# Performance work log

Measured on AMD Instinct MI355X. Metric: run time of the kernel, lower is better.

## Reference

```python
import jax, jax.numpy as jnp
import numpy as np

B, WK, HRS = 2048, 52, 8760
DT = 0.125          # Euler step in days (3-hourly), exactly representable
RANGE_PRED = 7      # forecast horizon in days


def setup_inputs() -> dict:
    key = jax.random.key(0)
    k1, k2, k3, k4 = jax.random.split(key, 4)
    # X_in: [B, weeks, 5, 1]; channel 0 = start time in days (same across batch,
    # the torch code reads X_in[0, week, 0, 0]); channels 1..4 = N,P,Z,D init.
    X_in = jax.random.uniform(k1, (B, WK, 5, 1), jnp.float32, 0.1, 3.0)
    t0 = jnp.arange(WK, dtype=jnp.float32) * 7.0
    X_in = X_in.at[:, :, 0, 0].set(jnp.broadcast_to(t0, (B, WK)))
    global_f = jax.random.uniform(k2, (B, HRS), jnp.float32)          # light forcing in [0,1]
    global_m = jax.random.uniform(k3, (B, HRS), jnp.float32) * 0.1    # mixing rate, small
    params_value = jax.random.uniform(k4, (B, 10), jnp.float32, 0.1, 1.0)
    return {"X_in": X_in, "global_f": global_f, "global_m": global_m,
            "params_value": params_value, "dt": DT, "range_pred": RANGE_PRED}


def reference(X_in, global_f, global_m, params_value, dt, range_pred):
    # Fixed multipliers from the torch code
    pv = jnp.asarray([1.0, 2.0, 0.1, 0.05, 0.1, 0.3, 0.6, 0.15, 0.4, 0.1], X_in.dtype)
    Q0, Vm, thr = 8.0, 1.0, 0.01  # Q0 = 4 + 2.5 + 1.5 + 0
    chi, rho, gam, lam, eps, alp, bet, eta, phi, zet = [params_value[:, i][:, None] for i in range(10)]  # [B,1]

    n_steps = int(round(range_pred / dt))      # 56
    stride = int(round(1.0 / dt))              # 8 -> daily sampling of output

    # Hourly forcing gather: same time axis for every batch element (torch uses X_in[0,...])
    t0 = X_in[0, :, 0, 0]                                                     # [W]
    times = t0[:, None] + jnp.arange(n_steps + 1, dtype=X_in.dtype) * dt      # [W, S]
    idx = jnp.round(times * 24.0).astype(jnp.int32)
    f = jnp.take(global_f, idx, axis=1)[:, :, :n_steps]                       # [B, W, T]
    m = jnp.take(global_m, idx, axis=1)[:, :, :n_steps]

    def step(carry, ft_mt):
        N, P, Z, D = carry                      # each [B, W]
        ft, mt = ft_mt
        Pc = jnp.maximum(thr, P)
        Zc = jnp.maximum(thr, Z)
        gN = N / (chi * pv[0] + N)
        zg = rho * pv[1] * (1.0 - jnp.exp(-lam * pv[3] * Pc)) * Zc
        up = Vm * gN * ft * Pc
        Nn = N + dt * (-up + alp * pv[5] * zg + eps * pv[4] * P + gam * pv[2] * Z + phi * pv[8] * D + mt * (Q0 - N))
        Pn = P + dt * (up - zg - eps * pv[4] * P - eta * pv[7] * P - mt * P)
        Zn = Z + dt * (bet * pv[6] * zg - gam * pv[2] * Z - mt * Z)
        Dn = D + dt * (eta * pv[7] * P + (1.0 - alp * pv[5] - bet * pv[6]) * zg - phi * pv[8] * D - zet * pv[9] * D - mt * D)
        new = (Nn, Pn, Zn, Dn)
        return new, jnp.stack(new, axis=0)      # [4, B, W]

    carry0 = (X_in[:, :, 1, 0], X_in[:, :, 2, 0], X_in[:, :, 3, 0], X_in[:, :, 4, 0])
    _, ys = jax.lax.scan(step, carry0, (jnp.moveaxis(f, 2, 0), jnp.moveaxis(m, 2, 0)))  # ys: [T, 4, B, W]
    traj = jnp.concatenate([jnp.stack(carry0, axis=0)[None], ys], axis=0)               # [S, 4, B, W]
    out = jnp.moveaxis(traj, (0, 1), (3, 2))                                            # [B, W, 4, S]
    return out[:, :, :, ::stride]               # daily samples: [B, W, 4, range_pred+1]
```

## Files before the change

### kernel.cpp

```cpp
#include <hip/hip_runtime.h>
#include <hip/hip_bf16.h>


#define NPZD_B 2048
#define NPZD_WK 52
#define NPZD_HRS 8760
#define NPZD_NSTEPS 56

__global__ __launch_bounds__(64) void npzd_kernel(
    const float* __restrict__ X_in,
    const float* __restrict__ gf,
    const float* __restrict__ gm,
    const float* __restrict__ params,
    const float* __restrict__ dt_ptr,
    float* __restrict__ out)
{
    const int t = blockIdx.x * blockDim.x + threadIdx.x;
    if (t >= NPZD_B * NPZD_WK) return;
    const int b = t / NPZD_WK;
    const int w = t - b * NPZD_WK;

    const float t0w = X_in[(size_t)w * 5];
    const int idx0 = (int)rintf(t0w * 24.0f);
    const float* __restrict__ frow = gf + (size_t)b * NPZD_HRS + idx0;
    const float* __restrict__ mrow = gm + (size_t)b * NPZD_HRS + idx0;

    float fv[NPZD_NSTEPS], mv[NPZD_NSTEPS];
    #pragma unroll
    for (int i = 0; i < NPZD_NSTEPS; ++i) fv[i] = frow[3 * i];
    #pragma unroll
    for (int i = 0; i < NPZD_NSTEPS; ++i) mv[i] = mrow[3 * i];

    const float dt = dt_ptr[0];

    const float* xb = X_in + (size_t)t * 5;
    float N = xb[1], P = xb[2], Z = xb[3], D = xb[4];

    const float* pp = params + (size_t)b * 10;
    const float chi   = pp[0];
    const float rho2  = pp[1] * 2.0f;
    const float gam1  = pp[2] * 0.1f;
    const float lam05 = pp[3] * 0.05f;
    const float eps1  = pp[4] * 0.1f;
    const float alp3  = pp[5] * 0.3f;
    const float bet6  = pp[6] * 0.6f;
    const float eta15 = pp[7] * 0.15f;
    const float phi4  = pp[8] * 0.4f;
    const float zet1  = pp[9] * 0.1f;
    const float rem   = 1.0f - alp3 - bet6;

    float oN[8], oP[8], oZ[8], oD[8];
    oN[0] = N; oP[0] = P; oZ[0] = Z; oD[0] = D;

    #pragma unroll
    for (int s = 0; s < NPZD_NSTEPS; ++s) {
        const float ft = fv[s], mt = mv[s];
        const float Pc = fmaxf(0.01f, P);
        const float Zc = fmaxf(0.01f, Z);
        const float gN = N / (chi + N);
        const float zg = rho2 * (1.0f - __expf(-lam05 * Pc)) * Zc;
        const float up = gN * ft * Pc;
        const float Nn = N + dt * (-up + alp3 * zg + eps1 * P + gam1 * Z + phi4 * D + mt * (8.0f - N));
        const float Pn = P + dt * (up - zg - eps1 * P - eta15 * P - mt * P);
        const float Zn = Z + dt * (bet6 * zg - gam1 * Z - mt * Z);
        const float Dn = D + dt * (eta15 * P + rem * zg - phi4 * D - zet1 * D - mt * D);
        N = Nn; P = Pn; Z = Zn; D = Dn;
        if ((s & 7) == 7) {
            const int c = (s >> 3) + 1;
            oN[c] = N; oP[c] = P; oZ[c] = Z; oD[c] = D;
        }
    }

    float4* o4 = (float4*)(out + (size_t)t * 32);
    o4[0] = make_float4(oN[0], oN[1], oN[2], oN[3]);
    o4[1] = make_float4(oN[4], oN[5], oN[6], oN[7]);
    o4[2] = make_float4(oP[0], oP[1], oP[2], oP[3]);
    o4[3] = make_float4(oP[4], oP[5], oP[6], oP[7]);
    o4[4] = make_float4(oZ[0], oZ[1], oZ[2], oZ[3]);
    o4[5] = make_float4(oZ[4], oZ[5], oZ[6], oZ[7]);
    o4[6] = make_float4(oD[0], oD[1], oD[2], oD[3]);
    o4[7] = make_float4(oD[4], oD[5], oD[6], oD[7]);
}

extern "C" void kernel_launch(void* const* d_in, const int* in_sizes, int n_in,
                              void* d_out, int out_size, void* d_ws, size_t ws_size,
                              hipStream_t stream) {
    const float* X_in   = (const float*)d_in[0];
    const float* gf     = (const float*)d_in[1];
    const float* gm     = (const float*)d_in[2];
    const float* params = (const float*)d_in[3];
    const float* dt_ptr = (const float*)d_in[4];
    float* out = (float*)d_out;

    const int n = NPZD_B * NPZD_WK;
    const int block = 64;
    const int grid = (n + block - 1) / block;
    npzd_kernel<<<grid, block, 0, stream>>>(X_in, gf, gm, params, dt_ptr, out);
}
```

Before: 187.3 us.

## Stage forcing gathers in LDS with one block per batch row

The kernel now launches one 256-thread block per batch element. All threads cooperatively gather the strided f and m forcing values for all 52 weeks into padded shared-memory arrays, then only 52 threads run the Euler integration, reading their forcing from LDS. This replaces per-thread strided global loads, which were uncoalesced across threads, with cooperative loads that are more spread across lanes. In exchange, about 80% of each block's threads sit idle during the serial integration phase, and the block now pays a barrier and LDS traffic.

New measurement: 182.2 us. 2.7% less time.

```diff
diff --git a/kernel.cpp b/kernel.cpp
--- a/kernel.cpp
+++ b/kernel.cpp
@@ -6,8 +6,10 @@
 #define NPZD_WK 52
 #define NPZD_HRS 8760
 #define NPZD_NSTEPS 56
+#define NPZD_PAD 57
+#define NPZD_NK (NPZD_WK * NPZD_NSTEPS)
 
-__global__ __launch_bounds__(64) void npzd_kernel(
+__global__ __launch_bounds__(256) void npzd_kernel(
     const float* __restrict__ X_in,
     const float* __restrict__ gf,
     const float* __restrict__ gm,
@@ -15,25 +17,40 @@
     const float* __restrict__ dt_ptr,
     float* __restrict__ out)
 {
-    const int t = blockIdx.x * blockDim.x + threadIdx.x;
-    if (t >= NPZD_B * NPZD_WK) return;
-    const int b = t / NPZD_WK;
-    const int w = t - b * NPZD_WK;
+    __shared__ float lds_f[NPZD_WK * NPZD_PAD];
+    __shared__ float lds_m[NPZD_WK * NPZD_PAD];
+    __shared__ int   lds_idx[NPZD_WK];
 
-    const float t0w = X_in[(size_t)w * 5];
-    const int idx0 = (int)rintf(t0w * 24.0f);
-    const float* __restrict__ frow = gf + (size_t)b * NPZD_HRS + idx0;
-    const float* __restrict__ mrow = gm + (size_t)b * NPZD_HRS + idx0;
+    const int b   = blockIdx.x;
+    const int tid = threadIdx.x;
 
-    float fv[NPZD_NSTEPS], mv[NPZD_NSTEPS];
+    if (tid < NPZD_WK) {
+        const float t0w = X_in[(size_t)tid * 5];
+        lds_idx[tid] = (int)rintf(t0w * 24.0f);
+    }
+    __syncthreads();
+
+    const float* __restrict__ frow = gf + (size_t)b * NPZD_HRS;
+    const float* __restrict__ mrow = gm + (size_t)b * NPZD_HRS;
     #pragma unroll
-    for (int i = 0; i < NPZD_NSTEPS; ++i) fv[i] = frow[3 * i];
-    #pragma unroll
-    for (int i = 0; i < NPZD_NSTEPS; ++i) mv[i] = mrow[3 * i];
+    for (int j = 0; j < (NPZD_NK + 255) / 256; ++j) {
+        const int k = tid + j * 256;
+        if (k < NPZD_NK) {
+            const int w = k / NPZD_NSTEPS;
+            const int s = k - w * NPZD_NSTEPS;
+            const int g = lds_idx[w] + 3 * s;
+            lds_f[w * NPZD_PAD + s] = frow[g];
+            lds_m[w * NPZD_PAD + s] = mrow[g];
+        }
+    }
+    __syncthreads();
+
+    if (tid >= NPZD_WK) return;
+    const int w = tid;
 
     const float dt = dt_ptr[0];
 
-    const float* xb = X_in + (size_t)t * 5;
+    const float* xb = X_in + ((size_t)b * NPZD_WK + w) * 5;
     float N = xb[1], P = xb[2], Z = xb[3], D = xb[4];
 
     const float* pp = params + (size_t)b * 10;
@@ -52,9 +69,12 @@
     float oN[8], oP[8], oZ[8], oD[8];
     oN[0] = N; oP[0] = P; oZ[0] = Z; oD[0] = D;
 
+    const float* lf = lds_f + w * NPZD_PAD;
+    const float* lm = lds_m + w * NPZD_PAD;
+
     #pragma unroll
     for (int s = 0; s < NPZD_NSTEPS; ++s) {
-        const float ft = fv[s], mt = mv[s];
+        const float ft = lf[s], mt = lm[s];
         const float Pc = fmaxf(0.01f, P);
         const float Zc = fmaxf(0.01f, Z);
         const float gN = N / (chi + N);
@@ -71,7 +91,7 @@
         }
     }
 
-    float4* o4 = (float4*)(out + (size_t)t * 32);
+    float4* o4 = (float4*)(out + ((size_t)b * NPZD_WK + w) * 32);
     o4[0] = make_float4(oN[0], oN[1], oN[2], oN[3]);
     o4[1] = make_float4(oN[4], oN[5], oN[6], oN[7]);
     o4[2] = make_float4(oP[0], oP[1], oP[2], oP[3]);
@@ -92,8 +112,5 @@
     const float* dt_ptr = (const float*)d_in[4];
     float* out = (float*)d_out;
 
-    const int n = NPZD_B * NPZD_WK;
-    const int block = 64;
-    const int grid = (n + block - 1) / block;
-    npzd_kernel<<<grid, block, 0, stream>>>(X_in, gf, gm, params, dt_ptr, out);
+    npzd_kernel<<<NPZD_B, 256, 0, stream>>>(X_in, gf, gm, params, dt_ptr, out);
 }
```
